# Performance work log

Measured on AMD Instinct MI355X. Metric: run time of the kernel, lower is better.

The kernel has to match this reference:

```python
import jax, jax.numpy as jnp
import numpy as np

D_MODEL = 1024
N_HEADS = 16


def setup_inputs() -> dict:
    key = jax.random.key(0)
    ks = jax.random.split(key, 7)
    scale = 1.0 / np.sqrt(D_MODEL)
    seq = jax.random.normal(ks[0], (4, 1024, D_MODEL), dtype=jnp.float32)
    Wq = jax.random.normal(ks[1], (D_MODEL, D_MODEL), dtype=jnp.float32) * scale
    bq = jax.random.normal(ks[2], (D_MODEL,), dtype=jnp.float32) * 0.02
    Wk = jax.random.normal(ks[3], (D_MODEL, D_MODEL), dtype=jnp.float32) * scale
    bk = jax.random.normal(ks[4], (D_MODEL,), dtype=jnp.float32) * 0.02
    Wv = jax.random.normal(ks[5], (D_MODEL, D_MODEL), dtype=jnp.float32) * scale
    bv = jax.random.normal(ks[6], (D_MODEL,), dtype=jnp.float32) * 0.02
    return {"seq": seq, "Wq": Wq, "bq": bq, "Wk": Wk, "bk": bk, "Wv": Wv, "bv": bv}


def reference(seq, Wq, bq, Wk, bk, Wv, bv):
    B, S, D = seq.shape
    H = N_HEADS
    dv = D // H
    # nn.Linear: x @ W.T + b; W stored [out, in]
    q = (seq @ Wq.T + bq).reshape(B, S, H, dv).transpose(0, 2, 1, 3)  # [B,H,S,dv]
    k = (seq @ Wk.T + bk).reshape(B, S, H, dv).transpose(0, 2, 1, 3)
    v = (seq @ Wv.T + bv).reshape(B, S, H, dv).transpose(0, 2, 1, 3)
    scores = jnp.einsum('bhqd,bhkd->bhqk', q, k) / jnp.sqrt(jnp.asarray(dv, seq.dtype))
    p = jax.nn.softmax(scores, axis=-1)
    out = jnp.einsum('bhqk,bhkd->bhqd', p, v)  # [B,H,S,dv]
    return out.transpose(0, 2, 1, 3).reshape(B, S, D)
```

## Files before the change

kernel.cpp:

```cpp
#include <hip/hip_runtime.h>
#include <hip/hip_fp16.h>

typedef _Float16 f16x8 __attribute__((ext_vector_type(8)));
typedef _Float16 f16x4 __attribute__((ext_vector_type(4)));
typedef float f32x4 __attribute__((ext_vector_type(4)));

#define D_MODEL 1024
#define SEQ 1024
#define BATCH 4
#define NH 16
#define DV 64
#define M_TOTAL (BATCH * SEQ)
#define QBLK 128

__device__ __forceinline__ void gload16(const _Float16* g, _Float16* lds) {
    __builtin_amdgcn_global_load_lds((const __attribute__((address_space(1))) void*)g,
                                     (__attribute__((address_space(3))) void*)lds,
                                     16, 0, 0);
}

__global__ void cvt_f32_f16(const float* __restrict__ s, _Float16* __restrict__ d, int n) {
    int i = (blockIdx.x * blockDim.x + threadIdx.x) * 8;
    if (i >= n) return;
    float4 a = *(const float4*)(s + i);
    float4 b = *(const float4*)(s + i + 4);
    f16x8 h;
    h[0] = (_Float16)a.x; h[1] = (_Float16)a.y; h[2] = (_Float16)a.z; h[3] = (_Float16)a.w;
    h[4] = (_Float16)b.x; h[5] = (_Float16)b.y; h[6] = (_Float16)b.z; h[7] = (_Float16)b.w;
    *(f16x8*)(d + i) = h;
}

__global__ void cvt3_f32_f16(const float* __restrict__ s0, const float* __restrict__ s1,
                             const float* __restrict__ s2, _Float16* __restrict__ d0,
                             _Float16* __restrict__ d1, _Float16* __restrict__ d2, int n) {
    const float* s = (blockIdx.y == 0) ? s0 : (blockIdx.y == 1 ? s1 : s2);
    _Float16*    d = (blockIdx.y == 0) ? d0 : (blockIdx.y == 1 ? d1 : d2);
    int i = (blockIdx.x * blockDim.x + threadIdx.x) * 8;
    if (i >= n) return;
    float4 a = *(const float4*)(s + i);
    float4 b = *(const float4*)(s + i + 4);
    f16x8 h;
    h[0] = (_Float16)a.x; h[1] = (_Float16)a.y; h[2] = (_Float16)a.z; h[3] = (_Float16)a.w;
    h[4] = (_Float16)b.x; h[5] = (_Float16)b.y; h[6] = (_Float16)b.z; h[7] = (_Float16)b.w;
    *(f16x8*)(d + i) = h;
}

__global__ __launch_bounds__(512, 2) void qkv_gemm(
    const _Float16* __restrict__ X,
    const _Float16* __restrict__ W0, const _Float16* __restrict__ W1, const _Float16* __restrict__ W2,
    const float* __restrict__ b0, const float* __restrict__ b1, const float* __restrict__ b2,
    _Float16* __restrict__ Qo, _Float16* __restrict__ Ko, _Float16* __restrict__ Vto)
{
    __shared__ _Float16 SM[4 * 256 * 64];
#define ABASE(buf) (SM + (buf) * 16384)
#define BBASE(buf) (SM + 32768 + (buf) * 16384)

    const int tid = threadIdx.x;
    const int l = tid & 63;
    const int w = tid >> 6;
    const int wr = w >> 2, wc = w & 3;

    const int bid = blockIdx.x;
    const int nid = (bid & 7) * 24 + (bid >> 3);
    const int mt = nid & 15, ntg = nid >> 4;
    const int mat = ntg >> 2, nt = ntg & 3;
    const _Float16* Wm  = (mat == 0) ? W0 : (mat == 1 ? W1 : W2);
    const float*    bia = (mat == 0) ? b0 : (mat == 1 ? b1 : b2);
    const int m0 = mt * 256, n0 = nt * 256;

    const int str = tid >> 3;
    const int sc8 = ((tid & 7) ^ (str & 7)) * 8;
    const _Float16* xsrc = X  + (size_t)(m0 + str) * D_MODEL + sc8;
    const _Float16* wsrc = Wm + (size_t)(n0 + str) * D_MODEL + sc8;
    const int ldst = str * 64 + (tid & 7) * 8;

#define SA(buf, kt, h) do { \
    gload16(xsrc + (size_t)((h) * 128) * D_MODEL + (kt) * 64, ABASE(buf) + (h) * 8192 + ldst); \
    gload16(xsrc + (size_t)((h) * 128 + 64) * D_MODEL + (kt) * 64, ABASE(buf) + (h) * 8192 + 4096 + ldst); } while (0)
#define SB(buf, kt, h) do { \
    gload16(wsrc + (size_t)((h) * 128) * D_MODEL + (kt) * 64, BBASE(buf) + (h) * 8192 + ldst); \
    gload16(wsrc + (size_t)((h) * 128 + 64) * D_MODEL + (kt) * 64, BBASE(buf) + (h) * 8192 + 4096 + ldst); } while (0)

    const int fr = l & 15, g = l >> 4, fr7 = l & 7;
    const int wrow = wr * 128, bcol = wc * 64;

    f32x4 acc[8][4] = {};
    f16x8 b[4][2];

    SB(0, 0, 0); SB(0, 0, 1);
    SA(0, 0, 0); SA(0, 0, 1);
    SB(1, 1, 0); SB(1, 1, 1);
    asm volatile("s_waitcnt vmcnt(4)" ::: "memory");
    __builtin_amdgcn_s_barrier();

#define PHASES(BUF, TSA_BUF, TSA, TSB_BUF, TSB)                                              \
    _Pragma("unroll")                                                                        \
    for (int p = 0; p < 4; ++p) {                                                            \
        if (p == 0) {                                                                        \
            _Pragma("unroll")                                                                \
            for (int nj = 0; nj < 4; ++nj) {                                                 \
                const int rb = (bcol + nj * 16 + fr) * 64;                                   \
                b[nj][0] = *(const f16x8*)&BBASE(BUF)[rb + ((g ^ fr7) << 3)];                \
                b[nj][1] = *(const f16x8*)&BBASE(BUF)[rb + (((4 + g) ^ fr7) << 3)];          \
            }                                                                                \
        }                                                                                    \
        f16x8 aq[2][2];                                                                      \
        _Pragma("unroll")                                                                    \
        for (int q = 0; q < 2; ++q) {                                                        \
            const int ra = (wrow + (2 * p + q) * 16 + fr) * 64;                              \
            aq[q][0] = *(const f16x8*)&ABASE(BUF)[ra + ((g ^ fr7) << 3)];                    \
            aq[q][1] = *(const f16x8*)&ABASE(BUF)[ra + (((4 + g) ^ fr7) << 3)];              \
        }                                                                                    \
        if (p == 0) SA(TSA_BUF, TSA, 0);                                                     \
        else if (p == 1) SA(TSA_BUF, TSA, 1);                                                \
        else if (p == 2) SB(TSB_BUF, TSB, 0);                                                \
        else SB(TSB_BUF, TSB, 1);                                                            \
        __builtin_amdgcn_s_barrier();                                                        \
        __builtin_amdgcn_s_setprio(1);                                                       \
        _Pragma("unroll")                                                                    \
        for (int ks = 0; ks < 2; ++ks)                                                       \
            _Pragma("unroll")                                                                \
            for (int q = 0; q < 2; ++q)                                                      \
                _Pragma("unroll")                                                            \
                for (int nj = 0; nj < 4; ++nj)                                               \
                    acc[2 * p + q][nj] = __builtin_amdgcn_mfma_f32_16x16x32_f16(             \
                        aq[q][ks], b[nj][ks], acc[2 * p + q][nj], 0, 0, 0);                  \
        __builtin_amdgcn_s_setprio(0);                                                       \
        if (p == 3) asm volatile("s_waitcnt vmcnt(4)" ::: "memory");                         \
        __builtin_amdgcn_s_barrier();                                                        \
    }

    for (int it = 0; it < 8; ++it) {
        const int tA = 2 * it + 1;
        const int tN = (2 * it + 2 < 16) ? 2 * it + 2 : 15;
        const int tM = (2 * it + 3 < 16) ? 2 * it + 3 : 15;
        PHASES(0, 1, tA, 0, tN)
        PHASES(1, 0, tN, 1, tM)
    }
#undef PHASES
#undef SA
#undef SB

    if (mat != 2) {
        const float scale = (mat == 0) ? 0.125f * 1.44269504088896340736f : 1.0f;
#pragma unroll
        for (int nj = 0; nj < 4; ++nj) {
            const int o = n0 + bcol + nj * 16 + fr;
            const float bb = bia[o];
            const int h = o >> 6, dd = o & 63;
#pragma unroll
            for (int mi = 0; mi < 8; ++mi) {
#pragma unroll
                for (int r = 0; r < 4; ++r) {
                    const int m = m0 + wrow + mi * 16 + g * 4 + r;
                    const int bi = m >> 10, s = m & 1023;
                    const float v = (acc[mi][nj][r] + bb) * scale;
                    const _Float16 hv = (_Float16)v;
                    const int bh = bi * NH + h;
                    if (mat == 0) Qo[((size_t)bh * SEQ + s) * DV + dd] = hv;
                    else          Ko[((size_t)bh * SEQ + s) * DV + dd] = hv;
                }
            }
        }
    } else {
        asm volatile("s_waitcnt vmcnt(0)" ::: "memory");
        __syncthreads();
#pragma unroll
        for (int nj = 0; nj < 4; ++nj) {
            const int n = bcol + nj * 16 + fr;
            const float bb = bia[n0 + n];
#pragma unroll
            for (int mi = 0; mi < 8; ++mi) {
#pragma unroll
                for (int r = 0; r < 4; ++r) {
                    const int m = wrow + mi * 16 + g * 4 + r;
                    SM[n * 256 + ((((m >> 3) + n) & 31) << 3) + (m & 7)] =
                        (_Float16)(acc[mi][nj][r] + bb);
                }
            }
        }
        __syncthreads();
        const int bi = m0 >> 10, s0 = m0 & 1023;
#pragma unroll
        for (int itp = 0; itp < 16; ++itp) {
            const int task = itp * 512 + tid;
            const int dd = task >> 5, sc = task & 31;
            f16x8 vv = *(const f16x8*)&SM[dd * 256 + (((sc + dd) & 31) << 3)];
            const int og = n0 + dd;
            const int h = og >> 6, d = og & 63;
            const int bh = bi * NH + h;
            *(f16x8*)(Vto + ((size_t)bh * DV + d) * SEQ + s0 + sc * 8) = vv;
        }
    }
#undef ABASE
#undef BBASE
}

__global__ __launch_bounds__(512, 4) void attn(
    const _Float16* __restrict__ Q, const _Float16* __restrict__ K,
    const _Float16* __restrict__ Vt, float* __restrict__ out)
{
    __shared__ _Float16 Kb[2][64 * 64];
    __shared__ _Float16 Vb[2][64 * 64];
    __shared__ _Float16 P[8][16][80];

    const int tid = threadIdx.x;
    const int w = tid >> 6, l = tid & 63;
    const int qc = l & 15, g = l >> 4;

    const int fid = blockIdx.y * 8 + blockIdx.x;
    const int nid = (fid & 7) * 64 + (fid >> 3);
    const int bh = nid >> 3, qt = nid & 7;
    const int b = bh >> 4, h = bh & 15;
    const int q0 = qt * QBLK + w * 16;

    const int str = tid >> 3;
    const int scs = ((tid & 7) ^ (str & 7)) * 8;
    const int ldst = str * 64 + (tid & 7) * 8;
    const _Float16* Kg = K  + (size_t)bh * SEQ * DV;
    const _Float16* Vg = Vt + (size_t)bh * DV * SEQ;

    const _Float16* qp = Q + ((size_t)bh * SEQ + q0 + qc) * DV + g * 8;
    f16x8 qf0 = *(const f16x8*)(qp);
    f16x8 qf1 = *(const f16x8*)(qp + 32);

    float m_run = -1e30f, l_run = 0.f;
    f32x4 oacc[4] = {};

#define STAGE(buf, kb) do {                                                  \
        gload16(Kg + (size_t)((kb) + str) * DV + scs, &Kb[buf][0] + ldst);   \
        gload16(Vg + (size_t)str * SEQ + (kb) + scs, &Vb[buf][0] + ldst);    \
    } while (0)

    STAGE(0, 0);
    __syncthreads();

    for (int kt = 0; kt < 16; ++kt) {
        const int ct = kt & 1;
        if (kt < 15) STAGE(ct ^ 1, (kt + 1) * 64);
        const _Float16* Ktile = Kb[ct];
        const _Float16* Vtile = Vb[ct];

        f32x4 sT[4];
        const f32x4 zf = {0.f, 0.f, 0.f, 0.f};
        __builtin_amdgcn_s_setprio(1);
#pragma unroll
        for (int kf = 0; kf < 4; ++kf) {
            const int row = kf * 16 + qc;
            f16x8 ka0 = *(const f16x8*)&Ktile[row * 64 + (((g)     ^ (qc & 7)) << 3)];
            f16x8 ka1 = *(const f16x8*)&Ktile[row * 64 + (((4 + g) ^ (qc & 7)) << 3)];
            f32x4 t = __builtin_amdgcn_mfma_f32_16x16x32_f16(ka0, qf0, zf, 0, 0, 0);
            sT[kf] = __builtin_amdgcn_mfma_f32_16x16x32_f16(ka1, qf1, t, 0, 0, 0);
        }
        __builtin_amdgcn_s_setprio(0);

        f32x4 mx = sT[0];
#pragma unroll
        for (int kf = 1; kf < 4; ++kf)
#pragma unroll
            for (int r = 0; r < 4; ++r) mx[r] = fmaxf(mx[r], sT[kf][r]);
        float pmax = fmaxf(fmaxf(mx[0], mx[1]), fmaxf(mx[2], mx[3]));
        pmax = fmaxf(pmax, __shfl_xor(pmax, 16));
        pmax = fmaxf(pmax, __shfl_xor(pmax, 32));
        if (!__all(pmax - m_run <= 8.0f)) {
            const float mn = fmaxf(m_run, pmax);
            const float al = exp2f(m_run - mn);
            l_run *= al;
#pragma unroll
            for (int df = 0; df < 4; ++df) oacc[df] *= al;
            m_run = mn;
        }
        float rsum = 0.f;
#pragma unroll
        for (int kf = 0; kf < 4; ++kf) {
            f16x4 ph;
#pragma unroll
            for (int r = 0; r < 4; ++r) {
                const float p = exp2f(sT[kf][r] - m_run);
                rsum += p;
                ph[r] = (_Float16)p;
            }
            *(f16x4*)&P[w][qc][kf * 16 + g * 4] = ph;
        }
        rsum += __shfl_xor(rsum, 16);
        rsum += __shfl_xor(rsum, 32);
        l_run += rsum;

        __builtin_amdgcn_s_setprio(1);
#pragma unroll
        for (int ks = 0; ks < 2; ++ks) {
            f16x8 pb = *(const f16x8*)&P[w][qc][ks * 32 + g * 8];
#pragma unroll
            for (int df = 0; df < 4; ++df) {
                const int row = df * 16 + qc;
                f16x8 va = *(const f16x8*)&Vtile[row * 64 + (((ks * 4 + g) ^ (qc & 7)) << 3)];
                oacc[df] = __builtin_amdgcn_mfma_f32_16x16x32_f16(va, pb, oacc[df], 0, 0, 0);
            }
        }
        __builtin_amdgcn_s_setprio(0);

        __syncthreads();
    }
#undef STAGE

    const float inv = 1.0f / l_run;
    float* ob = out + ((size_t)b * SEQ + q0 + qc) * D_MODEL + h * DV;
#pragma unroll
    for (int df = 0; df < 4; ++df) {
        float4 v4;
        v4.x = oacc[df][0] * inv; v4.y = oacc[df][1] * inv;
        v4.z = oacc[df][2] * inv; v4.w = oacc[df][3] * inv;
        *(float4*)(ob + df * 16 + g * 4) = v4;
    }
}

extern "C" void kernel_launch(void* const* d_in, const int* in_sizes, int n_in,
                              void* d_out, int out_size, void* d_ws, size_t ws_size,
                              hipStream_t stream) {
    const float* seq = (const float*)d_in[0];
    const float* Wq  = (const float*)d_in[1];
    const float* bq  = (const float*)d_in[2];
    const float* Wk  = (const float*)d_in[3];
    const float* bk  = (const float*)d_in[4];
    const float* Wv  = (const float*)d_in[5];
    const float* bv  = (const float*)d_in[6];
    float* out = (float*)d_out;

    _Float16* seqh = (_Float16*)d_ws;
    _Float16* wqh  = seqh + (size_t)M_TOTAL * D_MODEL;
    _Float16* wkh  = wqh + (size_t)D_MODEL * D_MODEL;
    _Float16* wvh  = wkh + (size_t)D_MODEL * D_MODEL;
    _Float16* Qh   = wvh + (size_t)D_MODEL * D_MODEL;
    _Float16* Kh   = Qh + (size_t)M_TOTAL * D_MODEL;
    _Float16* Vth  = Kh + (size_t)M_TOTAL * D_MODEL;

    const int n_seq = M_TOTAL * D_MODEL;
    const int n_w   = D_MODEL * D_MODEL;
    cvt_f32_f16<<<n_seq / (256 * 8), 256, 0, stream>>>(seq, seqh, n_seq);
    cvt3_f32_f16<<<dim3(n_w / (256 * 8), 3), 256, 0, stream>>>(Wq, Wk, Wv, wqh, wkh, wvh, n_w);

    qkv_gemm<<<192, 512, 0, stream>>>(
        seqh, wqh, wkh, wvh, bq, bk, bv, Qh, Kh, Vth);

    attn<<<dim3(SEQ / QBLK, BATCH * NH), 512, 0, stream>>>(Qh, Kh, Vth, out);
}
```

Measured before the change: 84.31 us.

## Use 32x32 MFMA attention with register-resident P and 4-wave blocks

Rewrites the attention kernel so each of 4 waves handles 32 query rows using 32x32 MFMA instructions. The QK^T result layout now matches the B-operand layout of the PV MFMA, so P stays in registers and the LDS round-trip for P is removed. The block shrinks from 512 to 256 threads, with each thread issuing twice the K/V staging loads. This trades more registers per thread and fewer waves per CU for fewer LDS accesses and larger MFMA tiles.

```diff
diff --git a/kernel.cpp b/kernel.cpp
--- a/kernel.cpp
+++ b/kernel.cpp
@@ -4,6 +4,7 @@
 typedef _Float16 f16x8 __attribute__((ext_vector_type(8)));
 typedef _Float16 f16x4 __attribute__((ext_vector_type(4)));
 typedef float f32x4 __attribute__((ext_vector_type(4)));
+typedef float f32x16 __attribute__((ext_vector_type(16)));
 
 #define D_MODEL 1024
 #define SEQ 1024
@@ -196,23 +197,22 @@
 #undef BBASE
 }
 
-__global__ __launch_bounds__(512, 4) void attn(
+__global__ __launch_bounds__(256, 2) void attn(
     const _Float16* __restrict__ Q, const _Float16* __restrict__ K,
     const _Float16* __restrict__ Vt, float* __restrict__ out)
 {
     __shared__ _Float16 Kb[2][64 * 64];
     __shared__ _Float16 Vb[2][64 * 64];
-    __shared__ _Float16 P[8][16][80];
 
     const int tid = threadIdx.x;
     const int w = tid >> 6, l = tid & 63;
-    const int qc = l & 15, g = l >> 4;
+    const int q_ = l & 31, hl = l >> 5;
 
     const int fid = blockIdx.y * 8 + blockIdx.x;
     const int nid = (fid & 7) * 64 + (fid >> 3);
     const int bh = nid >> 3, qt = nid & 7;
     const int b = bh >> 4, h = bh & 15;
-    const int q0 = qt * QBLK + w * 16;
+    const int q0 = qt * QBLK + w * 32;
 
     const int str = tid >> 3;
     const int scs = ((tid & 7) ^ (str & 7)) * 8;
@@ -220,97 +220,102 @@
     const _Float16* Kg = K  + (size_t)bh * SEQ * DV;
     const _Float16* Vg = Vt + (size_t)bh * DV * SEQ;
 
-    const _Float16* qp = Q + ((size_t)bh * SEQ + q0 + qc) * DV + g * 8;
-    f16x8 qf0 = *(const f16x8*)(qp);
-    f16x8 qf1 = *(const f16x8*)(qp + 32);
+    f16x8 qf[4];
+    {
+        const _Float16* qp = Q + ((size_t)bh * SEQ + q0 + q_) * DV + hl * 8;
+#pragma unroll
+        for (int c = 0; c < 4; ++c) qf[c] = *(const f16x8*)(qp + c * 16);
+    }
 
     float m_run = -1e30f, l_run = 0.f;
-    f32x4 oacc[4] = {};
-
-#define STAGE(buf, kb) do {                                                  \
-        gload16(Kg + (size_t)((kb) + str) * DV + scs, &Kb[buf][0] + ldst);   \
-        gload16(Vg + (size_t)str * SEQ + (kb) + scs, &Vb[buf][0] + ldst);    \
+    f32x16 acc0 = {}, acc1 = {};
+
+#define STAGE(buf, kt) do {                                                              \
+        gload16(Kg + (size_t)((kt) * 64 + str) * DV + scs, &Kb[buf][0] + ldst);          \
+        gload16(Kg + (size_t)((kt) * 64 + str + 32) * DV + scs, &Kb[buf][32 * 64] + ldst);\
+        gload16(Vg + (size_t)str * SEQ + (kt) * 64 + scs, &Vb[buf][0] + ldst);           \
+        gload16(Vg + (size_t)(str + 32) * SEQ + (kt) * 64 + scs, &Vb[buf][32 * 64] + ldst);\
+    } while (0)
+
+#define QK(S, ct, kt) do {                                                               \
+        S = (f32x16){};                                                                  \
+        const int row = (kt) * 32 + q_;                                                  \
+        _Pragma("unroll")                                                                \
+        for (int c = 0; c < 4; ++c) {                                                    \
+            f16x8 kf = *(const f16x8*)&Kb[ct][row * 64 + (((c * 2 + hl) ^ (row & 7)) << 3)]; \
+            S = __builtin_amdgcn_mfma_f32_32x32x16_f16(kf, qf[c], S, 0, 0, 0);           \
+        }                                                                                \
+    } while (0)
+
+#define SMPV(S, ct, kt) do {                                                             \
+        float lmax = S[0];                                                               \
+        _Pragma("unroll")                                                                \
+        for (int r = 1; r < 16; ++r) lmax = fmaxf(lmax, S[r]);                           \
+        const float mm = fmaxf(lmax, __shfl_xor(lmax, 32));                              \
+        if (!__all(mm - m_run <= 8.0f)) {                                                \
+            const float mn = fmaxf(m_run, mm);                                           \
+            const float al = exp2f(m_run - mn);                                          \
+            l_run *= al;                                                                 \
+            acc0 *= al; acc1 *= al;                                                      \
+            m_run = mn;                                                                  \
+        }                                                                                \
+        float p[16];                                                                     \
+        float rsum = 0.f;                                                                \
+        _Pragma("unroll")                                                                \
+        for (int r = 0; r < 16; ++r) { p[r] = exp2f(S[r] - m_run); rsum += p[r]; }       \
+        l_run += rsum;                                                                   \
+        f16x4 pf[4];                                                                     \
+        _Pragma("unroll")                                                                \
+        for (int G = 0; G < 4; ++G) {                                                    \
+            pf[G][0] = (_Float16)p[4 * G];     pf[G][1] = (_Float16)p[4 * G + 1];        \
+            pf[G][2] = (_Float16)p[4 * G + 2]; pf[G][3] = (_Float16)p[4 * G + 3];        \
+        }                                                                                \
+        __builtin_amdgcn_s_setprio(1);                                                   \
+        _Pragma("unroll")                                                                \
+        for (int G = 0; G < 4; ++G) {                                                    \
+            const int c16 = (kt) * 4 + G;                                                \
+            const int r0 = q_;                                                           \
+            f16x4 v0 = *(const f16x4*)&Vb[ct][r0 * 64 + (((c16) ^ (r0 & 7)) << 3) + hl * 4]; \
+            acc0 = __builtin_amdgcn_mfma_f32_32x32x8f16(v0, pf[G], acc0, 0, 0, 0);       \
+            const int r1 = 32 + q_;                                                      \
+            f16x4 v1 = *(const f16x4*)&Vb[ct][r1 * 64 + (((c16) ^ (r1 & 7)) << 3) + hl * 4]; \
+            acc1 = __builtin_amdgcn_mfma_f32_32x32x8f16(v1, pf[G], acc1, 0, 0, 0);       \
+        }                                                                                \
+        __builtin_amdgcn_s_setprio(0);                                                   \
     } while (0)
 
     STAGE(0, 0);
     __syncthreads();
 
-    for (int kt = 0; kt < 16; ++kt) {
-        const int ct = kt & 1;
-        if (kt < 15) STAGE(ct ^ 1, (kt + 1) * 64);
-        const _Float16* Ktile = Kb[ct];
-        const _Float16* Vtile = Vb[ct];
-
-        f32x4 sT[4];
-        const f32x4 zf = {0.f, 0.f, 0.f, 0.f};
-        __builtin_amdgcn_s_setprio(1);
-#pragma unroll
-        for (int kf = 0; kf < 4; ++kf) {
-            const int row = kf * 16 + qc;
-            f16x8 ka0 = *(const f16x8*)&Ktile[row * 64 + (((g)     ^ (qc & 7)) << 3)];
-            f16x8 ka1 = *(const f16x8*)&Ktile[row * 64 + (((4 + g) ^ (qc & 7)) << 3)];
-            f32x4 t = __builtin_amdgcn_mfma_f32_16x16x32_f16(ka0, qf0, zf, 0, 0, 0);
-            sT[kf] = __builtin_amdgcn_mfma_f32_16x16x32_f16(ka1, qf1, t, 0, 0, 0);
-        }
-        __builtin_amdgcn_s_setprio(0);
-
-        f32x4 mx = sT[0];
-#pragma unroll
-        for (int kf = 1; kf < 4; ++kf)
-#pragma unroll
-            for (int r = 0; r < 4; ++r) mx[r] = fmaxf(mx[r], sT[kf][r]);
-        float pmax = fmaxf(fmaxf(mx[0], mx[1]), fmaxf(mx[2], mx[3]));
-        pmax = fmaxf(pmax, __shfl_xor(pmax, 16));
-        pmax = fmaxf(pmax, __shfl_xor(pmax, 32));
-        if (!__all(pmax - m_run <= 8.0f)) {
-            const float mn = fmaxf(m_run, pmax);
-            const float al = exp2f(m_run - mn);
-            l_run *= al;
-#pragma unroll
-            for (int df = 0; df < 4; ++df) oacc[df] *= al;
-            m_run = mn;
-        }
-        float rsum = 0.f;
-#pragma unroll
-        for (int kf = 0; kf < 4; ++kf) {
-            f16x4 ph;
-#pragma unroll
-            for (int r = 0; r < 4; ++r) {
-                const float p = exp2f(sT[kf][r] - m_run);
-                rsum += p;
-                ph[r] = (_Float16)p;
-            }
-            *(f16x4*)&P[w][qc][kf * 16 + g * 4] = ph;
-        }
-        rsum += __shfl_xor(rsum, 16);
-        rsum += __shfl_xor(rsum, 32);
-        l_run += rsum;
-
-        __builtin_amdgcn_s_setprio(1);
-#pragma unroll
-        for (int ks = 0; ks < 2; ++ks) {
-            f16x8 pb = *(const f16x8*)&P[w][qc][ks * 32 + g * 8];
-#pragma unroll
-            for (int df = 0; df < 4; ++df) {
-                const int row = df * 16 + qc;
-                f16x8 va = *(const f16x8*)&Vtile[row * 64 + (((ks * 4 + g) ^ (qc & 7)) << 3)];
-                oacc[df] = __builtin_amdgcn_mfma_f32_16x16x32_f16(va, pb, oacc[df], 0, 0, 0);
-            }
-        }
-        __builtin_amdgcn_s_setprio(0);
+    for (int t = 0; t < 16; ++t) {
+        const int ct = t & 1;
+        if (t < 15) STAGE(ct ^ 1, t + 1);
+
+        f32x16 s0, s1;
+        QK(s0, ct, 0);
+        QK(s1, ct, 1);
+        SMPV(s0, ct, 0);
+        SMPV(s1, ct, 1);
 
         __syncthreads();
     }
 #undef STAGE
-
+#undef QK
+#undef SMPV
+
+    l_run += __shfl_xor(l_run, 32);
     const float inv = 1.0f / l_run;
-    float* ob = out + ((size_t)b * SEQ + q0 + qc) * D_MODEL + h * DV;
-#pragma unroll
-    for (int df = 0; df < 4; ++df) {
+    float* ob = out + ((size_t)b * SEQ + q0 + q_) * D_MODEL + h * DV;
+#pragma unroll
+    for (int rg = 0; rg < 4; ++rg) {
         float4 v4;
-        v4.x = oacc[df][0] * inv; v4.y = oacc[df][1] * inv;
-        v4.z = oacc[df][2] * inv; v4.w = oacc[df][3] * inv;
-        *(float4*)(ob + df * 16 + g * 4) = v4;
+        const int d0 = rg * 8 + 4 * hl;
+        v4.x = acc0[4 * rg + 0] * inv; v4.y = acc0[4 * rg + 1] * inv;
+        v4.z = acc0[4 * rg + 2] * inv; v4.w = acc0[4 * rg + 3] * inv;
+        *(float4*)(ob + d0) = v4;
+        v4.x = acc1[4 * rg + 0] * inv; v4.y = acc1[4 * rg + 1] * inv;
+        v4.z = acc1[4 * rg + 2] * inv; v4.w = acc1[4 * rg + 3] * inv;
+        *(float4*)(ob + 32 + d0) = v4;
     }
 }
 
@@ -342,5 +347,5 @@
     qkv_gemm<<<192, 512, 0, stream>>>(
         seqh, wqh, wkh, wvh, bq, bk, bv, Qh, Kh, Vth);
 
-    attn<<<dim3(SEQ / QBLK, BATCH * NH), 512, 0, stream>>>(Qh, Kh, Vth, out);
-}
+    attn<<<dim3(SEQ / QBLK, BATCH * NH), 256, 0, stream>>>(Qh, Kh, Vth, out);
+}
```

New measurement: 85.38 us. Within noise of the previous version (+1.3%).
